# Performance work log

Hardware: AMD Instinct MI355X
Metric: run time of the kernel (lower is better)

## Reference

```python
import jax, jax.numpy as jnp
import numpy as np

EPSILON = 1.0
SIGMA = 1.0
SPRING_K = 0.5
BATCH, NPART, DIM = 128, 512, 3


def setup_inputs() -> dict:
    key = jax.random.key(0)
    x = jax.random.normal(key, (BATCH, NPART, DIM), dtype=jnp.float32)
    return {"x": x}


def _remove_diag(d):
    # d: (B, N, N) -> (B, N, N-1), dropping the diagonal via the flatten trick
    B, N, _ = d.shape
    return d.reshape(B, N * N)[:, 1:].reshape(B, N - 1, N + 1)[:, :, :-1].reshape(B, N, N - 1)


def reference(x):
    # x: (B, N, D)
    B, N, D = x.shape
    pair_vec = x[:, :, None, :] - x[:, None, :, :]          # (B, N, N, D)
    distances = jnp.linalg.norm(pair_vec, axis=-1)           # (B, N, N)
    distances = _remove_diag(distances)                      # (B, N, N-1)
    distances_inverse = 1.0 / distances
    pow_6 = (SIGMA * distances_inverse) ** 6
    pair_potential = EPSILON * 4.0 * (pow_6 ** 2 - pow_6)
    pair_potential = pair_potential * distances_inverse * distances
    total_potential = jnp.sum(pair_potential, axis=(-1, -2)) / 2.0  # (B,)
    # harmonic restraint about center of mass (periodic=False branch)
    com = jnp.mean(x, axis=-2, keepdims=True)
    rel = x - com
    total_potential = total_potential + 0.5 * SPRING_K * jnp.sum(rel ** 2, axis=(-1, -2))
    # forward = log_prob = -potential
    return -total_potential
```

## Files before the change

kernel.cpp:

```cpp
#include <hip/hip_runtime.h>

#define NPART 512
#define BATCH 128


__global__ __launch_bounds__(1024, 4) void lj_main(
    const float* __restrict__ x, float* __restrict__ ws) {
    const int bid = blockIdx.x;
    const int b = bid >> 1;
    const int s = bid & 1;
    const int tid = threadIdx.x;
    const int t = tid & 127;
    const int h = tid >> 7;

    __shared__ float4 sp[768];
    __shared__ float wred[16];
    __shared__ float wspr[2][4];

    const float* xb = x + (size_t)b * (NPART * 3);
    float* spf = reinterpret_cast<float*>(sp);
    {
        const int idx = tid;
        const float v = xb[idx];
        const int p = idx / 3;
        const int c = idx - 3 * p;
        const int sl = (p & 3) * 192 + (p >> 2);
        spf[4 * sl + c] = v;
        if (p < 256) spf[4 * (sl + 128) + c] = v;
    }
    if (tid < 512) {
        const int idx = tid + 1024;
        const float v = xb[idx];
        const int p = idx / 3;
        const int c = idx - 3 * p;
        const int sl = (p & 3) * 192 + (p >> 2);
        spf[4 * sl + c] = v;
    }
    __syncthreads();

    const float4* R0 = sp + t;
    const float4* R1 = sp + 192 + t;
    const float4* R2 = sp + 384 + t;
    const float4* R3 = sp + 576 + t;

    const float4 pi0 = R0[0];
    const float4 pi1 = R1[0];
    const float4 pi2 = R2[0];
    const float4 pi3 = R3[0];

    const int X = 8 * s + h;
    const int B4 = 4 * X;

    float accA = 0.0f, accB = 0.0f;

    #define PT(PI, W, ACC) do {                                   \
        const float dx_ = (PI).x - (W).x;                         \
        const float dy_ = (PI).y - (W).y;                         \
        const float dz_ = (PI).z - (W).z;                         \
        const float r2_ = fmaf(dx_, dx_, fmaf(dy_, dy_, dz_ * dz_)); \
        const float i2_ = __builtin_amdgcn_rcpf(r2_);             \
        const float i6_ = i2_ * i2_ * i2_;                        \
        ACC = fmaf(i6_, i6_ - 1.0f, ACC);                         \
    } while (0)

    float4 w[19];
    w[0] = R1[B4];
    w[1] = R2[B4];
    w[2] = R3[B4];
    #pragma unroll
    for (int m = 0; m < 16; ++m) {
        const int q = B4 + 1 + (m >> 2);
        const int rg = m & 3;
        w[m + 3] = (rg == 0) ? R0[q] : (rg == 1) ? R1[q] : (rg == 2) ? R2[q] : R3[q];
        PT(pi0, w[m], accA);
        PT(pi1, w[m + 1], accA);
        PT(pi2, w[m + 2], accB);
        PT(pi3, w[m + 3], accB);
    }

    if (X == 15) {
        #define CORR(PI, W, ACC) do {                             \
            const float dx_ = (PI).x - (W).x;                     \
            const float dy_ = (PI).y - (W).y;                     \
            const float dz_ = (PI).z - (W).z;                     \
            const float r2_ = fmaf(dx_, dx_, fmaf(dy_, dy_, dz_ * dz_)); \
            const float i2_ = __builtin_amdgcn_rcpf(r2_);         \
            const float i6_ = i2_ * i2_ * i2_;                    \
            ACC -= 0.5f * i6_ * (i6_ - 1.0f);                     \
        } while (0)
        CORR(pi0, R0[64], accA);
        CORR(pi1, R1[64], accA);
        CORR(pi2, R2[64], accB);
        CORR(pi3, R3[64], accB);
        #undef CORR
    }
    #undef PT

    float pot = 4.0f * (accA + accB);

    #pragma unroll
    for (int off = 32; off; off >>= 1) pot += __shfl_down(pot, off, 64);

    float sx = 0.0f, sy = 0.0f, sz = 0.0f, ssq = 0.0f;
    if (X == 0) {
        sx = pi0.x + pi1.x + pi2.x + pi3.x;
        sy = pi0.y + pi1.y + pi2.y + pi3.y;
        sz = pi0.z + pi1.z + pi2.z + pi3.z;
        ssq = pi0.x * pi0.x + pi0.y * pi0.y + pi0.z * pi0.z
            + pi1.x * pi1.x + pi1.y * pi1.y + pi1.z * pi1.z
            + pi2.x * pi2.x + pi2.y * pi2.y + pi2.z * pi2.z
            + pi3.x * pi3.x + pi3.y * pi3.y + pi3.z * pi3.z;
        #pragma unroll
        for (int off = 32; off; off >>= 1) {
            sx  += __shfl_down(sx,  off, 64);
            sy  += __shfl_down(sy,  off, 64);
            sz  += __shfl_down(sz,  off, 64);
            ssq += __shfl_down(ssq, off, 64);
        }
    }

    const int wave = tid >> 6;
    const int lane = tid & 63;
    if (lane == 0) {
        wred[wave] = pot;
        if (wave < 2 && s == 0) {
            wspr[wave][0] = sx; wspr[wave][1] = sy;
            wspr[wave][2] = sz; wspr[wave][3] = ssq;
        }
    }
    __syncthreads();

    if (tid == 0) {
        float P = 0.0f;
        #pragma unroll
        for (int w2 = 0; w2 < 16; ++w2) P += wred[w2];
        float res = P;
        if (s == 0) {
            const float SX = wspr[0][0] + wspr[1][0];
            const float SY = wspr[0][1] + wspr[1][1];
            const float SZ = wspr[0][2] + wspr[1][2];
            const float SS = wspr[0][3] + wspr[1][3];
            res += 0.25f * (SS - (SX * SX + SY * SY + SZ * SZ) * (1.0f / NPART));
        }
        ws[bid] = res;
    }
}

__global__ void lj_combine(const float* __restrict__ ws,
                           float* __restrict__ out) {
    const int t = threadIdx.x;
    if (t < BATCH) out[t] = -(ws[2 * t] + ws[2 * t + 1]);
}

extern "C" void kernel_launch(void* const* d_in, const int* in_sizes, int n_in,
                              void* d_out, int out_size, void* d_ws, size_t ws_size,
                              hipStream_t stream) {
    const float* x = (const float*)d_in[0];
    float* out = (float*)d_out;
    float* pw = (float*)d_ws;

    lj_main<<<BATCH * 2, 1024, 0, stream>>>(x, pw);
    lj_combine<<<1, 128, 0, stream>>>(pw, out);
}
```

Measured before the change: 13.07 us.

## Pack pair math into float2 ops and share one reciprocal per pair

Moves shared memory from an AoS float4 layout to SoA per-coordinate arrays. The LJ inner loop now works on two partner particles at a time using packed float2 arithmetic, which maps to packed FP32 VALU instructions. A single rcp of r2a*r2b yields both inverse squared distances, halving the transcendental count. The risks are more shared-memory loads per pair, since x, y and z are loaded separately, and overflow or precision loss when the two r2 values are multiplied together.

```diff
diff --git a/kernel.cpp b/kernel.cpp
--- a/kernel.cpp
+++ b/kernel.cpp
@@ -1,4 +1,6 @@
 #include <hip/hip_runtime.h>
+
+typedef float v2f __attribute__((ext_vector_type(2)));
 
 #define NPART 512
 #define BATCH 128
@@ -13,103 +15,112 @@
     const int t = tid & 127;
     const int h = tid >> 7;
 
-    __shared__ float4 sp[768];
+    __shared__ float S[3][4][192];
     __shared__ float wred[16];
     __shared__ float wspr[2][4];
 
     const float* xb = x + (size_t)b * (NPART * 3);
-    float* spf = reinterpret_cast<float*>(sp);
     {
         const int idx = tid;
         const float v = xb[idx];
         const int p = idx / 3;
         const int c = idx - 3 * p;
-        const int sl = (p & 3) * 192 + (p >> 2);
-        spf[4 * sl + c] = v;
-        if (p < 256) spf[4 * (sl + 128) + c] = v;
+        S[c][p & 3][p >> 2] = v;
+        if (p < 256) S[c][p & 3][(p >> 2) + 128] = v;
     }
     if (tid < 512) {
         const int idx = tid + 1024;
         const float v = xb[idx];
         const int p = idx / 3;
         const int c = idx - 3 * p;
-        const int sl = (p & 3) * 192 + (p >> 2);
-        spf[4 * sl + c] = v;
+        S[c][p & 3][p >> 2] = v;
     }
     __syncthreads();
 
-    const float4* R0 = sp + t;
-    const float4* R1 = sp + 192 + t;
-    const float4* R2 = sp + 384 + t;
-    const float4* R3 = sp + 576 + t;
+    const int X = 8 * s + h;
+    const int tq = t + 4 * X;
 
-    const float4 pi0 = R0[0];
-    const float4 pi1 = R1[0];
-    const float4 pi2 = R2[0];
-    const float4 pi3 = R3[0];
+    const float pix0 = S[0][0][t], piy0 = S[1][0][t], piz0 = S[2][0][t];
+    const float pix1 = S[0][1][t], piy1 = S[1][1][t], piz1 = S[2][1][t];
+    const float pix2 = S[0][2][t], piy2 = S[1][2][t], piz2 = S[2][2][t];
+    const float pix3 = S[0][3][t], piy3 = S[1][3][t], piz3 = S[2][3][t];
 
-    const int X = 8 * s + h;
-    const int B4 = 4 * X;
+    const v2f px0 = {pix0, pix0}, py0 = {piy0, piy0}, pz0 = {piz0, piz0};
+    const v2f px1 = {pix1, pix1}, py1 = {piy1, piy1}, pz1 = {piz1, piz1};
+    const v2f px2 = {pix2, pix2}, py2 = {piy2, piy2}, pz2 = {piz2, piz2};
+    const v2f px3 = {pix3, pix3}, py3 = {piy3, piy3}, pz3 = {piz3, piz3};
 
-    float accA = 0.0f, accB = 0.0f;
+    v2f acc0 = {0.f, 0.f}, acc1 = {0.f, 0.f}, acc2 = {0.f, 0.f}, acc3 = {0.f, 0.f};
+    const v2f vone = {1.0f, 1.0f};
 
-    #define PT(PI, W, ACC) do {                                   \
-        const float dx_ = (PI).x - (W).x;                         \
-        const float dy_ = (PI).y - (W).y;                         \
-        const float dz_ = (PI).z - (W).z;                         \
-        const float r2_ = fmaf(dx_, dx_, fmaf(dy_, dy_, dz_ * dz_)); \
-        const float i2_ = __builtin_amdgcn_rcpf(r2_);             \
-        const float i6_ = i2_ * i2_ * i2_;                        \
-        ACC = fmaf(i6_, i6_ - 1.0f, ACC);                         \
+    #define PPK(r, XW, YW, ZW) do {                                        \
+        const v2f dX_ = px##r - (XW);                                      \
+        const v2f dY_ = py##r - (YW);                                      \
+        const v2f dZ_ = pz##r - (ZW);                                      \
+        const v2f R2_ = __builtin_elementwise_fma(dX_, dX_,                \
+                          __builtin_elementwise_fma(dY_, dY_, dZ_ * dZ_)); \
+        const float pr_ = R2_.x * R2_.y;                                   \
+        const float rt_ = __builtin_amdgcn_rcpf(pr_);                      \
+        v2f I2_; I2_.x = R2_.y * rt_; I2_.y = R2_.x * rt_;                 \
+        const v2f I6_ = I2_ * I2_ * I2_;                                   \
+        acc##r = __builtin_elementwise_fma(I6_, I6_ - vone, acc##r);       \
     } while (0)
 
-    float4 w[19];
-    w[0] = R1[B4];
-    w[1] = R2[B4];
-    w[2] = R3[B4];
-    #pragma unroll
-    for (int m = 0; m < 16; ++m) {
-        const int q = B4 + 1 + (m >> 2);
-        const int rg = m & 3;
-        w[m + 3] = (rg == 0) ? R0[q] : (rg == 1) ? R1[q] : (rg == 2) ? R2[q] : R3[q];
-        PT(pi0, w[m], accA);
-        PT(pi1, w[m + 1], accA);
-        PT(pi2, w[m + 2], accB);
-        PT(pi3, w[m + 3], accB);
+    #define LOADU(G, QC)                                                   \
+        v2f Xw; Xw.x = S[0][G][tq + (QC)]; Xw.y = S[0][G][tq + (QC) + 1];  \
+        v2f Yw; Yw.x = S[1][G][tq + (QC)]; Yw.y = S[1][G][tq + (QC) + 1];  \
+        v2f Zw; Zw.x = S[2][G][tq + (QC)]; Zw.y = S[2][G][tq + (QC) + 1];
+
+    { LOADU(1, 0) PPK(0, Xw, Yw, Zw); }
+    { LOADU(2, 0) PPK(0, Xw, Yw, Zw); PPK(1, Xw, Yw, Zw); }
+    { LOADU(3, 0) PPK(0, Xw, Yw, Zw); PPK(1, Xw, Yw, Zw); PPK(2, Xw, Yw, Zw); }
+    { LOADU(0, 1) PPK(0, Xw, Yw, Zw); PPK(1, Xw, Yw, Zw); PPK(2, Xw, Yw, Zw); PPK(3, Xw, Yw, Zw); }
+    { LOADU(1, 1) PPK(1, Xw, Yw, Zw); PPK(2, Xw, Yw, Zw); PPK(3, Xw, Yw, Zw); }
+    { LOADU(2, 1) PPK(2, Xw, Yw, Zw); PPK(3, Xw, Yw, Zw); }
+    { LOADU(3, 1) PPK(3, Xw, Yw, Zw); }
+    { LOADU(1, 2) PPK(0, Xw, Yw, Zw); }
+    { LOADU(2, 2) PPK(0, Xw, Yw, Zw); PPK(1, Xw, Yw, Zw); }
+    { LOADU(3, 2) PPK(0, Xw, Yw, Zw); PPK(1, Xw, Yw, Zw); PPK(2, Xw, Yw, Zw); }
+    { LOADU(0, 3) PPK(0, Xw, Yw, Zw); PPK(1, Xw, Yw, Zw); PPK(2, Xw, Yw, Zw); PPK(3, Xw, Yw, Zw); }
+    { LOADU(1, 3) PPK(1, Xw, Yw, Zw); PPK(2, Xw, Yw, Zw); PPK(3, Xw, Yw, Zw); }
+    { LOADU(2, 3) PPK(2, Xw, Yw, Zw); PPK(3, Xw, Yw, Zw); }
+    { LOADU(3, 3) PPK(3, Xw, Yw, Zw); }
+    #undef LOADU
+    #undef PPK
+
+    float corr = 0.0f;
+    if (X == 15) {
+        #define CORR(r) do {                                               \
+            const float wx = S[0][r][t + 64];                              \
+            const float wy = S[1][r][t + 64];                              \
+            const float wz = S[2][r][t + 64];                              \
+            const float dx_ = pix##r - wx;                                 \
+            const float dy_ = piy##r - wy;                                 \
+            const float dz_ = piz##r - wz;                                 \
+            const float r2_ = fmaf(dx_, dx_, fmaf(dy_, dy_, dz_ * dz_));   \
+            const float i2_ = __builtin_amdgcn_rcpf(r2_);                  \
+            const float i6_ = i2_ * i2_ * i2_;                             \
+            corr -= 0.5f * i6_ * (i6_ - 1.0f);                             \
+        } while (0)
+        CORR(0); CORR(1); CORR(2); CORR(3);
+        #undef CORR
     }
 
-    if (X == 15) {
-        #define CORR(PI, W, ACC) do {                             \
-            const float dx_ = (PI).x - (W).x;                     \
-            const float dy_ = (PI).y - (W).y;                     \
-            const float dz_ = (PI).z - (W).z;                     \
-            const float r2_ = fmaf(dx_, dx_, fmaf(dy_, dy_, dz_ * dz_)); \
-            const float i2_ = __builtin_amdgcn_rcpf(r2_);         \
-            const float i6_ = i2_ * i2_ * i2_;                    \
-            ACC -= 0.5f * i6_ * (i6_ - 1.0f);                     \
-        } while (0)
-        CORR(pi0, R0[64], accA);
-        CORR(pi1, R1[64], accA);
-        CORR(pi2, R2[64], accB);
-        CORR(pi3, R3[64], accB);
-        #undef CORR
-    }
-    #undef PT
-
-    float pot = 4.0f * (accA + accB);
+    float pot = 4.0f * (acc0.x + acc0.y + acc1.x + acc1.y +
+                        acc2.x + acc2.y + acc3.x + acc3.y + corr);
 
     #pragma unroll
     for (int off = 32; off; off >>= 1) pot += __shfl_down(pot, off, 64);
 
     float sx = 0.0f, sy = 0.0f, sz = 0.0f, ssq = 0.0f;
     if (X == 0) {
-        sx = pi0.x + pi1.x + pi2.x + pi3.x;
-        sy = pi0.y + pi1.y + pi2.y + pi3.y;
-        sz = pi0.z + pi1.z + pi2.z + pi3.z;
-        ssq = pi0.x * pi0.x + pi0.y * pi0.y + pi0.z * pi0.z
-            + pi1.x * pi1.x + pi1.y * pi1.y + pi1.z * pi1.z
-            + pi2.x * pi2.x + pi2.y * pi2.y + pi2.z * pi2.z
-            + pi3.x * pi3.x + pi3.y * pi3.y + pi3.z * pi3.z;
+        sx = pix0 + pix1 + pix2 + pix3;
+        sy = piy0 + piy1 + piy2 + piy3;
+        sz = piz0 + piz1 + piz2 + piz3;
+        ssq = pix0 * pix0 + piy0 * piy0 + piz0 * piz0
+            + pix1 * pix1 + piy1 * piy1 + piz1 * piz1
+            + pix2 * pix2 + piy2 * piy2 + piz2 * piz2
+            + pix3 * pix3 + piy3 * piy3 + piz3 * piz3;
         #pragma unroll
         for (int off = 32; off; off >>= 1) {
             sx  += __shfl_down(sx,  off, 64);
```

After: 13.54 us. +3.6%, slower.
